# Kernel tuning notes

Hardware: AMD Instinct MI355X
Metric: run time of the kernel (lower is better)

The kernel has to match this reference:

```python
import jax, jax.numpy as jnp
import numpy as np

MASK_VAL = -1e30


def setup_inputs() -> dict:
    key = jax.random.key(0)
    ks = jax.random.split(key, 9)
    B, C, Q, D = 64, 2048, 128, 128
    s = 0.05  # small param init scale (xavier-like)
    return {
        "vfeats": jax.random.normal(ks[0], (B, C, D), jnp.float32),
        "qfeats": jax.random.normal(ks[1], (B, Q, D), jnp.float32),
        "vmask": jnp.ones((B, C), jnp.float32),
        "qmask": jnp.ones((B, Q), jnp.float32),
        "w4C": jax.random.normal(ks[2], (D, 1), jnp.float32) * s,
        "w4Q": jax.random.normal(ks[3], (D, 1), jnp.float32) * s,
        "w4mlu": jax.random.normal(ks[4], (1, 1, D), jnp.float32) * s,
        "cqa_W": jax.random.normal(ks[5], (D, 4 * D), jnp.float32) * s,  # Conv1D k=1 == Linear(4D->D)
        "cqa_b": jnp.zeros((D,), jnp.float32),
        "wp": jax.random.normal(ks[6], (D, 1), jnp.float32) * s,
        "cc_W": jax.random.normal(ks[7], (D, 2 * D), jnp.float32) * s,  # Conv1D k=1 == Linear(2D->D)
        "cc_b": jnp.zeros((D,), jnp.float32),
    }


def reference(vfeats, qfeats, vmask, qmask, w4C, w4Q, w4mlu, cqa_W, cqa_b, wp, cc_W, cc_b):
    # --- CQAttention ---
    # trilinear score: [B, C, Q]  (dropout is identity at inference)
    score = (vfeats @ w4C) \
        + jnp.swapaxes(qfeats @ w4Q, 1, 2) \
        + jnp.einsum('bcd,bqd->bcq', vfeats * w4mlu, qfeats)
    score_ = jax.nn.softmax(score + (1.0 - qmask[:, None, :]) * MASK_VAL, axis=2)   # [B,C,Q]
    score_t = jax.nn.softmax(score + (1.0 - vmask[:, :, None]) * MASK_VAL, axis=1)  # [B,C,Q]
    c2q = score_ @ qfeats                                                           # [B,C,D]
    # q2c = (score_ @ score_t^T) @ context; reassociate to avoid the [B,C,C] matrix
    q2c = score_ @ jnp.einsum('bcq,bcd->bqd', score_t, vfeats)                      # [B,C,D]
    cat = jnp.concatenate([vfeats, c2q, vfeats * c2q, vfeats * q2c], axis=2)        # [B,C,4D]
    feats = cat @ cqa_W.T + cqa_b                                                   # [B,C,D]
    # --- CQConcatenate (weighted pool of query) ---
    alpha = jax.nn.softmax((qfeats @ wp) + (1.0 - qmask[:, :, None]) * MASK_VAL, axis=1)  # [B,Q,1]
    pooled = jnp.einsum('bqd,bq->bd', qfeats, alpha[..., 0])                        # [B,D]
    pooled = jnp.broadcast_to(pooled[:, None, :], feats.shape)                      # [B,C,D]
    out = jnp.concatenate([feats, pooled], axis=2) @ cc_W.T + cc_b                  # [B,C,D]
    return jax.nn.relu(out)
```

## Files before the change

kernel.cpp:

```cpp
#include <hip/hip_runtime.h>
#include <stdint.h>

#define DI __device__ __forceinline__

typedef __attribute__((ext_vector_type(8))) short short8;
typedef __attribute__((ext_vector_type(4))) short short4v;
typedef __attribute__((ext_vector_type(4))) float float4v;
typedef __attribute__((ext_vector_type(2))) float float2v;
typedef __attribute__((ext_vector_type(4))) unsigned int uint4v;
typedef __attribute__((ext_vector_type(2))) unsigned int uint2v;
typedef __attribute__((ext_vector_type(2))) __bf16 bf162;

#define MFMA16(a, b, c) __builtin_amdgcn_mfma_f32_16x16x32_bf16((a), (b), (c), 0, 0, 0)

DI float b2f(short s) {
    uint32_t u = ((uint32_t)(uint16_t)s) << 16;
    float f;
    __builtin_memcpy(&f, &u, 4);
    return f;
}
DI unsigned int cvtpk(float a, float b) {
    bf162 h = __builtin_convertvector((float2v){a, b}, bf162);
    return __builtin_bit_cast(unsigned int, h);
}
DI short f2b(float f) { return (short)__builtin_bit_cast(unsigned short, (__bf16)f); }
DI float u2f(unsigned int u) { return __builtin_bit_cast(float, u); }


__global__ __launch_bounds__(256) void k_packfuse(const float* __restrict__ src, const float* __restrict__ wm,
                                                  const float* __restrict__ wv, const float* __restrict__ mask,
                                                  short* __restrict__ dstA, short* __restrict__ dstT,
                                                  float* __restrict__ dotout, int nkc) {
    __shared__ float St[32 * 133];
    int t = threadIdx.x, kc = blockIdx.x, b = blockIdx.y;
    int rl = t >> 3, sub = t & 7, dseg = sub * 16;
    int grow = (b * nkc + kc) * 32 + rl;
    const float* p = src + ((size_t)grow << 7) + dseg;
    float4v v[4];
#pragma unroll
    for (int g = 0; g < 4; ++g) v[g] = *(const float4v*)(p + g * 4);
    float s = 0.f;
#pragma unroll
    for (int g = 0; g < 4; ++g) {
        float4v wg = *(const float4v*)(wv + dseg + g * 4);
#pragma unroll
        for (int j = 0; j < 4; ++j) s += v[g][j] * wg[j];
    }
#pragma unroll
    for (int off = 1; off < 8; off <<= 1) s += __shfl_xor(s, off, 64);
    if (sub == 0) dotout[grow] = s + (1.f - mask[grow]) * (-1e30f);
#pragma unroll
    for (int g = 0; g < 4; ++g)
#pragma unroll
        for (int j = 0; j < 4; ++j) St[rl * 133 + dseg + g * 4 + j] = v[g][j];
#pragma unroll
    for (int h = 0; h < 2; ++h) {
        int c16 = sub * 2 + h;
        int ks = c16 >> 2, quad = c16 & 3;
        float4v m0 = wm ? *(const float4v*)(wm + c16 * 8) : (float4v){1.f, 1.f, 1.f, 1.f};
        float4v m1 = wm ? *(const float4v*)(wm + c16 * 8 + 4) : (float4v){1.f, 1.f, 1.f, 1.f};
        uint4v ou;
        ou[0] = cvtpk(v[h * 2][0] * m0[0], v[h * 2][1] * m0[1]);
        ou[1] = cvtpk(v[h * 2][2] * m0[2], v[h * 2][3] * m0[3]);
        ou[2] = cvtpk(v[h * 2 + 1][0] * m1[0], v[h * 2 + 1][1] * m1[1]);
        ou[3] = cvtpk(v[h * 2 + 1][2] * m1[2], v[h * 2 + 1][3] * m1[3]);
        int tile = b * (nkc * 2) + kc * 2 + (rl >> 4);
        *(short8*)(dstA + ((size_t)(tile * 4 + ks) << 9) + (quad * 16 + (rl & 15)) * 8) =
            __builtin_bit_cast(short8, ou);
    }
    __syncthreads();
#pragma unroll
    for (int i = 0; i < 2; ++i) {
        int dt = (t >> 6) + i * 4;
        int lane = t & 63, ln = lane & 15, quad = lane >> 4;
        int d = dt * 16 + ln;
        uint4v ou;
#pragma unroll
        for (int wd = 0; wd < 4; ++wd)
            ou[wd] = cvtpk(St[(quad * 8 + 2 * wd) * 133 + d], St[(quad * 8 + 2 * wd + 1) * 133 + d]);
        *(short8*)(dstT + (((size_t)(b * 8 + dt) * nkc + kc) << 9) + lane * 8) = __builtin_bit_cast(short8, ou);
    }
}

__global__ __launch_bounds__(256) void k_packW(const float* __restrict__ wsrc, short* __restrict__ dst) {
    int idx = blockIdx.x * 256 + threadIdx.x;
    int lane = idx & 63, ks = (idx >> 6) & 3, part = (idx >> 8) & 3, nt = idx >> 10;
    const float* p = wsrc + (size_t)(nt * 16 + (lane & 15)) * 512 + part * 128 + ks * 32 + (lane >> 4) * 8;
    float4v a = *(const float4v*)p, b = *(const float4v*)(p + 4);
    uint4v ou;
    ou[0] = cvtpk(a[0], a[1]);
    ou[1] = cvtpk(a[2], a[3]);
    ou[2] = cvtpk(b[0], b[1]);
    ou[3] = cvtpk(b[2], b[3]);
    *(short8*)(dst + (size_t)idx * 8) = __builtin_bit_cast(short8, ou);
}

__global__ __launch_bounds__(256) void k_packWc(const float* __restrict__ wsrc, short* __restrict__ dst) {
    int idx = blockIdx.x * 256 + threadIdx.x;
    int lane = idx & 63, ks = (idx >> 6) & 3, ot = idx >> 8;
    const float* p = wsrc + (size_t)(ot * 16 + (lane & 15)) * 256 + ks * 32 + (lane >> 4) * 8;
    float4v a = *(const float4v*)p, b = *(const float4v*)(p + 4);
    uint4v ou;
    ou[0] = cvtpk(a[0], a[1]);
    ou[1] = cvtpk(a[2], a[3]);
    ou[2] = cvtpk(b[0], b[1]);
    ou[3] = cvtpk(b[2], b[3]);
    *(short8*)(dst + (size_t)idx * 8) = __builtin_bit_cast(short8, ou);
}

__global__ __launch_bounds__(128) void k_pool(const float* __restrict__ qf, const float* __restrict__ qmask,
                                              const float* __restrict__ wp, const float* __restrict__ ccW,
                                              const float* __restrict__ ccb, float* __restrict__ pc) {
    __shared__ float tmp[128], af[128], pooled[128];
    int b = blockIdx.x, t = threadIdx.x;
    const float* qrow = qf + ((size_t)(b * 128 + t) << 7);
    float s = 0.f;
    for (int d = 0; d < 128; ++d) s += qrow[d] * wp[d];
    s += (1.f - qmask[b * 128 + t]) * (-1e30f);
    tmp[t] = s;
    __syncthreads();
    for (int off = 64; off >= 1; off >>= 1) {
        if (t < off) tmp[t] = fmaxf(tmp[t], tmp[t + off]);
        __syncthreads();
    }
    float m = tmp[0];
    __syncthreads();
    float e = __expf(s - m);
    tmp[t] = e;
    __syncthreads();
    for (int off = 64; off >= 1; off >>= 1) {
        if (t < off) tmp[t] += tmp[t + off];
        __syncthreads();
    }
    af[t] = e / tmp[0];
    __syncthreads();
    float p = 0.f;
    for (int q = 0; q < 128; ++q) p += qf[((size_t)(b * 128 + q) << 7) + t] * af[q];
    pooled[t] = p;
    __syncthreads();
    float acc = ccb[t];
    for (int d = 0; d < 128; ++d) acc += pooled[d] * ccW[t * 256 + 128 + d];
    pc[b * 128 + t] = acc;
}

__global__ __launch_bounds__(256) void k_Tacc(const short* __restrict__ vfA, const short* __restrict__ vfT,
                                              const short* __restrict__ qfBW, const float* __restrict__ cvp,
                                              float* __restrict__ Pg, float* __restrict__ Csg) {
    __shared__ short Al[16 * 136];
    __shared__ float Red[4][16][130];
    __shared__ float csred[4][16];
    int tid = threadIdx.x, w = tid >> 6, lane = tid & 63, ln = lane & 15, quad = lane >> 4;
    int id = blockIdx.x;
    int xcd = id & 7, k = id >> 3;
    int g = xcd * 16 + (k & 15);
    int qt = k >> 4;
    int b = g & 63, s = g >> 6;
    short8 bq[4];
#pragma unroll
    for (int ks = 0; ks < 4; ++ks) bq[ks] = *(const short8*)(qfBW + (((size_t)(b * 8 + qt) * 4 + ks) << 9) + lane * 8);
    float4v acc[8];
#pragma unroll
    for (int dt = 0; dt < 8; ++dt) acc[dt] = (float4v){0.f, 0.f, 0.f, 0.f};
    float colacc = 0.f;
    for (int it = 0; it < 8; ++it) {
        int cbase = s * 1024 + it * 128 + w * 32;
        int ct = b * 128 + (cbase >> 4);
        float4v ds[2];
        ds[0] = (float4v){0.f, 0.f, 0.f, 0.f};
        ds[1] = (float4v){0.f, 0.f, 0.f, 0.f};
#pragma unroll
        for (int ks = 0; ks < 4; ++ks) {
#pragma unroll
            for (int mt = 0; mt < 2; ++mt) {
                short8 a = *(const short8*)(vfA + (((size_t)(ct + mt) * 4 + ks) << 9) + lane * 8);
                ds[mt] = MFMA16(a, bq[ks], ds[mt]);
            }
        }
#pragma unroll
        for (int mt = 0; mt < 2; ++mt) {
            float4v cv = *(const float4v*)(cvp + b * 2048 + cbase + mt * 16 + quad * 4);
            float e0 = __expf(ds[mt][0] + cv[0]);
            float e1 = __expf(ds[mt][1] + cv[1]);
            float e2 = __expf(ds[mt][2] + cv[2]);
            float e3 = __expf(ds[mt][3] + cv[3]);
            colacc += e0 + e1 + e2 + e3;
            uint2v eu;
            eu[0] = cvtpk(e0, e1);
            eu[1] = cvtpk(e2, e3);
            *(short4v*)(Al + ln * 136 + w * 32 + mt * 16 + quad * 4) = __builtin_bit_cast(short4v, eu);
        }
        short8 a = *(const short8*)(Al + ln * 136 + w * 32 + quad * 8);
#pragma unroll
        for (int dt = 0; dt < 8; ++dt) {
            short8 bb = *(const short8*)(vfT + (((size_t)(b * 8 + dt) * 64 + s * 32 + it * 4 + w) << 9) + lane * 8);
            acc[dt] = MFMA16(a, bb, acc[dt]);
        }
    }
#pragma unroll
    for (int dt = 0; dt < 8; ++dt)
#pragma unroll
        for (int r = 0; r < 4; ++r) Red[w][quad * 4 + r][dt * 16 + ln] = acc[dt][r];
    float p = colacc;
    p += __shfl_xor(p, 16, 64);
    p += __shfl_xor(p, 32, 64);
    if (lane < 16) csred[w][lane] = p;
    __syncthreads();
    if (tid < 16)
        Csg[((size_t)(s * 64 + b)) * 128 + qt * 16 + tid] =
            csred[0][tid] + csred[1][tid] + csred[2][tid] + csred[3][tid];
    {
        int q = tid >> 4, db = (tid & 15) * 8;
        float4v s0, s1;
#pragma unroll
        for (int j = 0; j < 4; ++j) {
            s0[j] = Red[0][q][db + j] + Red[1][q][db + j] + Red[2][q][db + j] + Red[3][q][db + j];
            s1[j] = Red[0][q][db + 4 + j] + Red[1][q][db + 4 + j] + Red[2][q][db + 4 + j] + Red[3][q][db + 4 + j];
        }
        size_t pb = (((size_t)(s * 64 + b)) * 8 + qt) * 2048 + q * 128 + db;
        *(float4v*)(Pg + pb) = s0;
        *(float4v*)(Pg + pb + 4) = s1;
    }
}

__global__ __launch_bounds__(256) void k_Tcomb(const float* __restrict__ Pg, const float* __restrict__ Csg,
                                               short* __restrict__ Ttf) {
    int idx = blockIdx.x * 256 + threadIdx.x;
    int lane = idx & 63, dt = (idx >> 8) & 7, b = idx >> 11;
    int d = dt * 16 + (lane & 15), q0 = ((idx >> 6) & 3) * 32 + (lane >> 4) * 8;
    float pv[8];
#pragma unroll
    for (int j = 0; j < 8; ++j) {
        int q = q0 + j;
        size_t o0 = ((size_t)(b * 8) + (q >> 4)) * 2048 + (q & 15) * 128 + d;
        size_t o1 = ((size_t)((64 + b) * 8) + (q >> 4)) * 2048 + (q & 15) * 128 + d;
        float cs = Csg[b * 128 + q] + Csg[(64 + b) * 128 + q];
        pv[j] = (Pg[o0] + Pg[o1]) * __builtin_amdgcn_rcpf(cs);
    }
    uint4v ou;
#pragma unroll
    for (int wd = 0; wd < 4; ++wd) ou[wd] = cvtpk(pv[2 * wd], pv[2 * wd + 1]);
    *(short8*)(Ttf + (size_t)idx * 8) = __builtin_bit_cast(short8, ou);
}

__global__ __launch_bounds__(256, 4) void k_out(const short* __restrict__ vfA, const short* __restrict__ qfBW,
                                                const short* __restrict__ qTf, const short* __restrict__ Ttf,
                                                const float* __restrict__ qvp, const short* __restrict__ cqaWp,
                                                const float* __restrict__ cqab, const short* __restrict__ ccWp,
                                                const float* __restrict__ pc, float* __restrict__ out) {
    __shared__ __align__(16) short Sl[64 * 128];
    __shared__ __align__(16) short Xl[64 * 128];
    int tid = threadIdx.x, w = tid >> 6, lane = tid & 63, ln = lane & 15, quad = lane >> 4;
    int jl = ln & 7, hi8 = ln >> 3;
    int id = blockIdx.x;
    int xcd = id & 7, k = id >> 3;
    int b = xcd * 8 + (k & 7);
    int cx = k >> 3;
    int c0 = cx * 64 + w * 16;
    int tt = b * 128 + (c0 >> 4);
    int wbase = w * 2048;
    {
        float4v sc[8];
#pragma unroll
        for (int qt = 0; qt < 8; ++qt) sc[qt] = (float4v){0.f, 0.f, 0.f, 0.f};
#pragma unroll
        for (int ks = 0; ks < 4; ++ks) {
            short8 av = *(const short8*)(vfA + (((size_t)tt * 4 + ks) << 9) + lane * 8);
#pragma unroll
            for (int qt = 0; qt < 8; ++qt) {
                short8 bq = *(const short8*)(qfBW + (((size_t)(b * 8 + qt) * 4 + ks) << 9) + lane * 8);
                sc[qt] = MFMA16(av, bq, sc[qt]);
            }
        }
        float qvl[8];
#pragma unroll
        for (int qt = 0; qt < 8; ++qt) qvl[qt] = qvp[b * 128 + qt * 16 + ln];
#pragma unroll
        for (int r = 0; r < 4; ++r) {
            float x[8], m = -3.4e38f;
#pragma unroll
            for (int qt = 0; qt < 8; ++qt) {
                x[qt] = sc[qt][r] + qvl[qt];
                m = fmaxf(m, x[qt]);
            }
#pragma unroll
            for (int off = 1; off < 16; off <<= 1) m = fmaxf(m, __shfl_xor(m, off, 64));
            float e[8], sm = 0.f;
#pragma unroll
            for (int qt = 0; qt < 8; ++qt) {
                e[qt] = __expf(x[qt] - m);
                sm += e[qt];
            }
#pragma unroll
            for (int off = 1; off < 16; off <<= 1) sm += __shfl_xor(sm, off, 64);
            float inv = __builtin_amdgcn_rcpf(sm);
            int rb = (quad * 4 + r) * 8 + jl;
#pragma unroll
            for (int qp = 0; qp < 4; ++qp) {
                unsigned int u = cvtpk(e[2 * qp] * inv, e[2 * qp + 1] * inv);
                Sl[wbase + qp * 512 + hi8 * 128 + rb] = (short)u;
                Sl[wbase + qp * 512 + (2 + hi8) * 128 + rb] = (short)(u >> 16);
            }
        }
    }
    {
        float4v a2q[8];
#pragma unroll
        for (int dt = 0; dt < 8; ++dt) a2q[dt] = (float4v){0.f, 0.f, 0.f, 0.f};
#pragma unroll
        for (int ks = 0; ks < 4; ++ks) {
            short8 a = *(const short8*)(Sl + wbase + ks * 512 + lane * 8);
#pragma unroll
            for (int dt = 0; dt < 8; ++dt) {
                short8 b1 = *(const short8*)(qTf + (((size_t)(b * 8 + dt) * 4 + ks) << 9) + lane * 8);
                a2q[dt] = MFMA16(a, b1, a2q[dt]);
            }
        }
#pragma unroll
        for (int r = 0; r < 4; ++r) {
            int rb = (quad * 4 + r) * 8 + jl;
#pragma unroll
            for (int dp = 0; dp < 4; ++dp) {
                unsigned int u = cvtpk(a2q[2 * dp][r], a2q[2 * dp + 1][r]);
                Xl[wbase + dp * 512 + hi8 * 128 + rb] = (short)u;
                Xl[wbase + dp * 512 + (2 + hi8) * 128 + rb] = (short)(u >> 16);
            }
        }
    }
    {
        float4v aq2[8];
#pragma unroll
        for (int dt = 0; dt < 8; ++dt) aq2[dt] = (float4v){0.f, 0.f, 0.f, 0.f};
#pragma unroll
        for (int ks = 0; ks < 4; ++ks) {
            short8 a = *(const short8*)(Sl + wbase + ks * 512 + lane * 8);
#pragma unroll
            for (int dt = 0; dt < 8; ++dt) {
                short8 b2 = *(const short8*)(Ttf + (((size_t)(b * 8 + dt) * 4 + ks) << 9) + lane * 8);
                aq2[dt] = MFMA16(a, b2, aq2[dt]);
            }
        }
#pragma unroll
        for (int r = 0; r < 4; ++r) {
            int rb = (quad * 4 + r) * 8 + jl;
#pragma unroll
            for (int dp = 0; dp < 4; ++dp) {
                unsigned int u = cvtpk(aq2[2 * dp][r], aq2[2 * dp + 1][r]);
                Sl[wbase + dp * 512 + hi8 * 128 + rb] = (short)u;
                Sl[wbase + dp * 512 + (2 + hi8) * 128 + rb] = (short)(u >> 16);
            }
        }
    }
    __syncthreads();
    float4v accF[4][2];
#pragma unroll
    for (int ct = 0; ct < 4; ++ct)
#pragma unroll
        for (int nt2 = 0; nt2 < 2; ++nt2) accF[ct][nt2] = (float4v){0.f, 0.f, 0.f, 0.f};
#pragma unroll
    for (int ks = 0; ks < 4; ++ks) {
        short8 avk[4];
#pragma unroll
        for (int ct = 0; ct < 4; ++ct)
            avk[ct] = *(const short8*)(vfA + (((size_t)(b * 128 + cx * 4 + ct) * 4 + ks) << 9) + lane * 8);
#pragma unroll
        for (int part = 0; part < 4; ++part) {
            short8 bwp[2];
#pragma unroll
            for (int nt2 = 0; nt2 < 2; ++nt2)
                bwp[nt2] =
                    *(const short8*)(cqaWp + (((size_t)((w * 2 + nt2) * 4 + part) * 4 + ks) << 9) + lane * 8);
            short8 a[4];
#pragma unroll
            for (int ct = 0; ct < 4; ++ct) {
                int fo = ct * 2048 + ks * 512 + lane * 8;
                if (part == 0) {
                    a[ct] = avk[ct];
                } else if (part == 1) {
                    a[ct] = *(const short8*)(Xl + fo);
                } else {
                    short8 mfr = (part == 2) ? *(const short8*)(Xl + fo) : *(const short8*)(Sl + fo);
                    uint4v ua = __builtin_bit_cast(uint4v, avk[ct]);
                    uint4v um = __builtin_bit_cast(uint4v, mfr);
                    uint4v uo;
#pragma unroll
                    for (int wd = 0; wd < 4; ++wd) {
                        float a0 = u2f(ua[wd] << 16), a1 = u2f(ua[wd] & 0xffff0000u);
                        float m0 = u2f(um[wd] << 16), m1 = u2f(um[wd] & 0xffff0000u);
                        uo[wd] = cvtpk(a0 * m0, a1 * m1);
                    }
                    a[ct] = __builtin_bit_cast(short8, uo);
                }
            }
#pragma unroll
            for (int nt2 = 0; nt2 < 2; ++nt2)
#pragma unroll
                for (int ct = 0; ct < 4; ++ct) accF[ct][nt2] = MFMA16(a[ct], bwp[nt2], accF[ct][nt2]);
        }
    }
    __syncthreads();
    {
        float b0 = cqab[(w * 2) * 16 + ln], b1 = cqab[(w * 2 + 1) * 16 + ln];
#pragma unroll
        for (int ct = 0; ct < 4; ++ct)
#pragma unroll
            for (int r = 0; r < 4; ++r) {
                unsigned int u = cvtpk(accF[ct][0][r] + b0, accF[ct][1][r] + b1);
                int rb = ct * 2048 + w * 512 + (quad * 4 + r) * 8 + jl;
                Sl[rb + hi8 * 128] = (short)u;
                Sl[rb + (2 + hi8) * 128] = (short)(u >> 16);
            }
    }
    __syncthreads();
    float4v accO[4][2];
#pragma unroll
    for (int ct = 0; ct < 4; ++ct)
#pragma unroll
        for (int ot2 = 0; ot2 < 2; ++ot2) accO[ct][ot2] = (float4v){0.f, 0.f, 0.f, 0.f};
#pragma unroll
    for (int ks = 0; ks < 4; ++ks) {
        short8 bwo[2];
#pragma unroll
        for (int ot2 = 0; ot2 < 2; ++ot2)
            bwo[ot2] = *(const short8*)(ccWp + (((size_t)((w * 2 + ot2) * 4 + ks)) << 9) + lane * 8);
        short8 a[4];
#pragma unroll
        for (int ct = 0; ct < 4; ++ct) a[ct] = *(const short8*)(Sl + ct * 2048 + ks * 512 + lane * 8);
#pragma unroll
        for (int ot2 = 0; ot2 < 2; ++ot2)
#pragma unroll
            for (int ct = 0; ct < 4; ++ct) accO[ct][ot2] = MFMA16(a[ct], bwo[ot2], accO[ct][ot2]);
    }
#pragma unroll
    for (int ct = 0; ct < 4; ++ct)
#pragma unroll
        for (int ot2 = 0; ot2 < 2; ++ot2) {
            int o = (w * 2 + ot2) * 16 + ln;
            float pco = pc[b * 128 + o];
#pragma unroll
            for (int r = 0; r < 4; ++r) {
                int c = cx * 64 + ct * 16 + quad * 4 + r;
                out[((size_t)(b * 2048 + c) << 7) + o] = fmaxf(accO[ct][ot2][r] + pco, 0.f);
            }
        }
}

extern "C" void kernel_launch(void* const* d_in, const int* in_sizes, int n_in, void* d_out, int out_size, void* d_ws,
                              size_t ws_size, hipStream_t stream) {
    const float* vf = (const float*)d_in[0];
    const float* qf = (const float*)d_in[1];
    const float* vmask = (const float*)d_in[2];
    const float* qmask = (const float*)d_in[3];
    const float* w4C = (const float*)d_in[4];
    const float* w4Q = (const float*)d_in[5];
    const float* w4mlu = (const float*)d_in[6];
    const float* cqaW = (const float*)d_in[7];
    const float* cqab = (const float*)d_in[8];
    const float* wp = (const float*)d_in[9];
    const float* ccW = (const float*)d_in[10];
    const float* ccb = (const float*)d_in[11];
    float* out = (float*)d_out;
    char* ws = (char*)d_ws;

    size_t o = 0;
    short* vfA = (short*)(ws + o); o += 64ull * 2048 * 128 * 2;
    short* vfT = (short*)(ws + o); o += 64ull * 2048 * 128 * 2;
    short* qfBW = (short*)(ws + o); o += 64ull * 128 * 128 * 2;
    short* qTf = (short*)(ws + o); o += 64ull * 128 * 128 * 2;
    short* Ttf = (short*)(ws + o); o += 64ull * 128 * 128 * 2;
    short* cqaWp = (short*)(ws + o); o += 128ull * 512 * 2;
    short* ccWp = (short*)(ws + o); o += 128ull * 128 * 2;
    float* Pg = (float*)(ws + o); o += 2ull * 64 * 128 * 128 * 4;
    float* Csg = (float*)(ws + o); o += 2ull * 64 * 128 * 4;
    float* cvp = (float*)(ws + o); o += 64ull * 2048 * 4;
    float* qvp = (float*)(ws + o); o += 64ull * 128 * 4;
    float* pc = (float*)(ws + o); o += 64ull * 128 * 4;

    k_packfuse<<<dim3(64, 64), 256, 0, stream>>>(vf, nullptr, w4C, vmask, vfA, vfT, cvp, 64);
    k_packfuse<<<dim3(4, 64), 256, 0, stream>>>(qf, w4mlu, w4Q, qmask, qfBW, qTf, qvp, 4);
    k_packW<<<32, 256, 0, stream>>>(cqaW, cqaWp);
    k_packWc<<<8, 256, 0, stream>>>(ccW, ccWp);
    k_pool<<<64, 128, 0, stream>>>(qf, qmask, wp, ccW, ccb, pc);
    k_Tacc<<<1024, 256, 0, stream>>>(vfA, vfT, qfBW, cvp, Pg, Csg);
    k_Tcomb<<<512, 256, 0, stream>>>(Pg, Csg, Ttf);
    k_out<<<2048, 256, 0, stream>>>(vfA, qfBW, qTf, Ttf, qvp, cqaWp, cqab, ccWp, pc, out);
}
```

Measured before the change: 286.1 us.

## Merge prep kernels into fewer launches and prefetch MFMA operands earlier

The two packfuse launches are merged into one grid that branches on block index, and the weight-pack and pooling kernels are merged into one k_small launch. This cuts the launch count from eight to five. The pooling part now uses 256 threads with vectorized loads and split reductions. In k_Tacc and k_out, the B-operand loads are hoisted ahead of the MFMA loops behind sched_barriers to hide global load latency, at the cost of higher register pressure.

```diff
diff --git a/kernel.cpp b/kernel.cpp
--- a/kernel.cpp
+++ b/kernel.cpp
@@ -23,16 +23,34 @@
     bf162 h = __builtin_convertvector((float2v){a, b}, bf162);
     return __builtin_bit_cast(unsigned int, h);
 }
-DI short f2b(float f) { return (short)__builtin_bit_cast(unsigned short, (__bf16)f); }
 DI float u2f(unsigned int u) { return __builtin_bit_cast(float, u); }
 
 
-__global__ __launch_bounds__(256) void k_packfuse(const float* __restrict__ src, const float* __restrict__ wm,
-                                                  const float* __restrict__ wv, const float* __restrict__ mask,
-                                                  short* __restrict__ dstA, short* __restrict__ dstT,
-                                                  float* __restrict__ dotout, int nkc) {
+__global__ __launch_bounds__(256) void k_packfuse(const float* __restrict__ vf, const float* __restrict__ qf,
+                                                  const float* __restrict__ w4C, const float* __restrict__ w4Q,
+                                                  const float* __restrict__ w4mlu, const float* __restrict__ vmask,
+                                                  const float* __restrict__ qmask, short* __restrict__ vfA,
+                                                  short* __restrict__ vfT, short* __restrict__ qfBW,
+                                                  short* __restrict__ qTf, float* __restrict__ cvp,
+                                                  float* __restrict__ qvp) {
     __shared__ float St[32 * 133];
-    int t = threadIdx.x, kc = blockIdx.x, b = blockIdx.y;
+    int bx = blockIdx.x, b = blockIdx.y;
+    const float* src;
+    const float* wm;
+    const float* wv;
+    const float* mask;
+    short* dstA;
+    short* dstT;
+    float* dotout;
+    int kc, nkc;
+    if (bx < 64) {
+        src = vf; wm = nullptr; wv = w4C; mask = vmask;
+        dstA = vfA; dstT = vfT; dotout = cvp; kc = bx; nkc = 64;
+    } else {
+        src = qf; wm = w4mlu; wv = w4Q; mask = qmask;
+        dstA = qfBW; dstT = qTf; dotout = qvp; kc = bx - 64; nkc = 4;
+    }
+    int t = threadIdx.x;
     int rl = t >> 3, sub = t & 7, dseg = sub * 16;
     int grow = (b * nkc + kc) * 32 + rl;
     const float* p = src + ((size_t)grow << 7) + dseg;
@@ -82,42 +100,52 @@
     }
 }
 
-__global__ __launch_bounds__(256) void k_packW(const float* __restrict__ wsrc, short* __restrict__ dst) {
-    int idx = blockIdx.x * 256 + threadIdx.x;
-    int lane = idx & 63, ks = (idx >> 6) & 3, part = (idx >> 8) & 3, nt = idx >> 10;
-    const float* p = wsrc + (size_t)(nt * 16 + (lane & 15)) * 512 + part * 128 + ks * 32 + (lane >> 4) * 8;
-    float4v a = *(const float4v*)p, b = *(const float4v*)(p + 4);
-    uint4v ou;
-    ou[0] = cvtpk(a[0], a[1]);
-    ou[1] = cvtpk(a[2], a[3]);
-    ou[2] = cvtpk(b[0], b[1]);
-    ou[3] = cvtpk(b[2], b[3]);
-    *(short8*)(dst + (size_t)idx * 8) = __builtin_bit_cast(short8, ou);
-}
-
-__global__ __launch_bounds__(256) void k_packWc(const float* __restrict__ wsrc, short* __restrict__ dst) {
-    int idx = blockIdx.x * 256 + threadIdx.x;
-    int lane = idx & 63, ks = (idx >> 6) & 3, ot = idx >> 8;
-    const float* p = wsrc + (size_t)(ot * 16 + (lane & 15)) * 256 + ks * 32 + (lane >> 4) * 8;
-    float4v a = *(const float4v*)p, b = *(const float4v*)(p + 4);
-    uint4v ou;
-    ou[0] = cvtpk(a[0], a[1]);
-    ou[1] = cvtpk(a[2], a[3]);
-    ou[2] = cvtpk(b[0], b[1]);
-    ou[3] = cvtpk(b[2], b[3]);
-    *(short8*)(dst + (size_t)idx * 8) = __builtin_bit_cast(short8, ou);
-}
-
-__global__ __launch_bounds__(128) void k_pool(const float* __restrict__ qf, const float* __restrict__ qmask,
-                                              const float* __restrict__ wp, const float* __restrict__ ccW,
-                                              const float* __restrict__ ccb, float* __restrict__ pc) {
-    __shared__ float tmp[128], af[128], pooled[128];
-    int b = blockIdx.x, t = threadIdx.x;
-    const float* qrow = qf + ((size_t)(b * 128 + t) << 7);
+__global__ __launch_bounds__(256) void k_small(const float* __restrict__ cqaW, short* __restrict__ cqaWp,
+                                               const float* __restrict__ ccW, short* __restrict__ ccWp,
+                                               const float* __restrict__ qf, const float* __restrict__ qmask,
+                                               const float* __restrict__ wp, const float* __restrict__ ccb,
+                                               float* __restrict__ pc) {
+    int bid = blockIdx.x, t = threadIdx.x;
+    if (bid < 32) {
+        int idx = bid * 256 + t;
+        int lane = idx & 63, ks = (idx >> 6) & 3, part = (idx >> 8) & 3, nt = idx >> 10;
+        const float* p = cqaW + (size_t)(nt * 16 + (lane & 15)) * 512 + part * 128 + ks * 32 + (lane >> 4) * 8;
+        float4v a = *(const float4v*)p, b = *(const float4v*)(p + 4);
+        uint4v ou;
+        ou[0] = cvtpk(a[0], a[1]);
+        ou[1] = cvtpk(a[2], a[3]);
+        ou[2] = cvtpk(b[0], b[1]);
+        ou[3] = cvtpk(b[2], b[3]);
+        *(short8*)(cqaWp + (size_t)idx * 8) = __builtin_bit_cast(short8, ou);
+        return;
+    }
+    if (bid < 40) {
+        int idx = (bid - 32) * 256 + t;
+        int lane = idx & 63, ks = (idx >> 6) & 3, ot = idx >> 8;
+        const float* p = ccW + (size_t)(ot * 16 + (lane & 15)) * 256 + ks * 32 + (lane >> 4) * 8;
+        float4v a = *(const float4v*)p, b = *(const float4v*)(p + 4);
+        uint4v ou;
+        ou[0] = cvtpk(a[0], a[1]);
+        ou[1] = cvtpk(a[2], a[3]);
+        ou[2] = cvtpk(b[0], b[1]);
+        ou[3] = cvtpk(b[2], b[3]);
+        *(short8*)(ccWp + (size_t)idx * 8) = __builtin_bit_cast(short8, ou);
+        return;
+    }
+    __shared__ float tmp[128], af[128], pp[2][128], pooled[128];
+    int b = bid - 40;
+    int q = t >> 1, hf = t & 1;
+    const float* qrow = qf + ((size_t)(b * 128 + q) << 7) + hf * 64;
     float s = 0.f;
-    for (int d = 0; d < 128; ++d) s += qrow[d] * wp[d];
-    s += (1.f - qmask[b * 128 + t]) * (-1e30f);
-    tmp[t] = s;
+#pragma unroll 4
+    for (int d = 0; d < 64; d += 4) {
+        float4v xv = *(const float4v*)(qrow + d);
+        float4v wg = *(const float4v*)(wp + hf * 64 + d);
+        s += xv[0] * wg[0] + xv[1] * wg[1] + xv[2] * wg[2] + xv[3] * wg[3];
+    }
+    s += __shfl_xor(s, 1, 64);
+    s += (1.f - qmask[b * 128 + q]) * (-1e30f);
+    if (hf == 0) tmp[q] = s;
     __syncthreads();
     for (int off = 64; off >= 1; off >>= 1) {
         if (t < off) tmp[t] = fmaxf(tmp[t], tmp[t + off]);
@@ -126,21 +154,31 @@
     float m = tmp[0];
     __syncthreads();
     float e = __expf(s - m);
-    tmp[t] = e;
+    if (hf == 0) tmp[q] = e;
     __syncthreads();
     for (int off = 64; off >= 1; off >>= 1) {
         if (t < off) tmp[t] += tmp[t + off];
         __syncthreads();
     }
-    af[t] = e / tmp[0];
-    __syncthreads();
-    float p = 0.f;
-    for (int q = 0; q < 128; ++q) p += qf[((size_t)(b * 128 + q) << 7) + t] * af[q];
-    pooled[t] = p;
-    __syncthreads();
-    float acc = ccb[t];
-    for (int d = 0; d < 128; ++d) acc += pooled[d] * ccW[t * 256 + 128 + d];
-    pc[b * 128 + t] = acc;
+    if (hf == 0) af[q] = e * __builtin_amdgcn_rcpf(tmp[0]);
+    __syncthreads();
+    {
+        int d = t & 127, qh = t >> 7;
+        float pacc = 0.f;
+        for (int qq = qh * 64; qq < qh * 64 + 64; ++qq) pacc += qf[((size_t)(b * 128 + qq) << 7) + d] * af[qq];
+        pp[qh][d] = pacc;
+    }
+    __syncthreads();
+    if (t < 128) pooled[t] = pp[0][t] + pp[1][t];
+    __syncthreads();
+    {
+        int o = t & 127, dh = t >> 7;
+        float acc = 0.f;
+        for (int d = dh * 64; d < dh * 64 + 64; ++d) acc += pooled[d] * ccW[o * 256 + 128 + d];
+        pp[dh][o] = acc;
+    }
+    __syncthreads();
+    if (t < 128) pc[b * 128 + t] = ccb[t] + pp[0][t] + pp[1][t];
 }
 
 __global__ __launch_bounds__(256) void k_Tacc(const short* __restrict__ vfA, const short* __restrict__ vfT,
@@ -165,6 +203,11 @@
     for (int it = 0; it < 8; ++it) {
         int cbase = s * 1024 + it * 128 + w * 32;
         int ct = b * 128 + (cbase >> 4);
+        short8 bb[4];
+#pragma unroll
+        for (int dt = 0; dt < 4; ++dt)
+            bb[dt] = *(const short8*)(vfT + (((size_t)(b * 8 + dt) * 64 + s * 32 + it * 4 + w) << 9) + lane * 8);
+        __builtin_amdgcn_sched_barrier(0);
         float4v ds[2];
         ds[0] = (float4v){0.f, 0.f, 0.f, 0.f};
         ds[1] = (float4v){0.f, 0.f, 0.f, 0.f};
@@ -191,9 +234,11 @@
         }
         short8 a = *(const short8*)(Al + ln * 136 + w * 32 + quad * 8);
 #pragma unroll
-        for (int dt = 0; dt < 8; ++dt) {
-            short8 bb = *(const short8*)(vfT + (((size_t)(b * 8 + dt) * 64 + s * 32 + it * 4 + w) << 9) + lane * 8);
-            acc[dt] = MFMA16(a, bb, acc[dt]);
+        for (int dt = 0; dt < 4; ++dt) acc[dt] = MFMA16(a, bb[dt], acc[dt]);
+#pragma unroll
+        for (int dt = 4; dt < 8; ++dt) {
+            short8 b2 = *(const short8*)(vfT + (((size_t)(b * 8 + dt) * 64 + s * 32 + it * 4 + w) << 9) + lane * 8);
+            acc[dt] = MFMA16(a, b2, acc[dt]);
         }
     }
 #pragma unroll
@@ -251,6 +296,7 @@
     __shared__ __align__(16) short Xl[64 * 128];
     int tid = threadIdx.x, w = tid >> 6, lane = tid & 63, ln = lane & 15, quad = lane >> 4;
     int jl = ln & 7, hi8 = ln >> 3;
+    const float4v z4 = {0.f, 0.f, 0.f, 0.f};
     int id = blockIdx.x;
     int xcd = id & 7, k = id >> 3;
     int b = xcd * 8 + (k & 7);
@@ -261,19 +307,25 @@
     {
         float4v sc[8];
 #pragma unroll
-        for (int qt = 0; qt < 8; ++qt) sc[qt] = (float4v){0.f, 0.f, 0.f, 0.f};
+        for (int qt = 0; qt < 8; ++qt) sc[qt] = z4;
 #pragma unroll
         for (int ks = 0; ks < 4; ++ks) {
+            short8 bqf[8];
+#pragma unroll
+            for (int qt = 0; qt < 8; ++qt)
+                bqf[qt] = *(const short8*)(qfBW + (((size_t)(b * 8 + qt) * 4 + ks) << 9) + lane * 8);
             short8 av = *(const short8*)(vfA + (((size_t)tt * 4 + ks) << 9) + lane * 8);
 #pragma unroll
-            for (int qt = 0; qt < 8; ++qt) {
-                short8 bq = *(const short8*)(qfBW + (((size_t)(b * 8 + qt) * 4 + ks) << 9) + lane * 8);
-                sc[qt] = MFMA16(av, bq, sc[qt]);
-            }
+            for (int qt = 0; qt < 8; ++qt) sc[qt] = MFMA16(av, bqf[qt], sc[qt]);
         }
         float qvl[8];
 #pragma unroll
         for (int qt = 0; qt < 8; ++qt) qvl[qt] = qvp[b * 128 + qt * 16 + ln];
+        short8 p2[8];
+#pragma unroll
+        for (int dt = 0; dt < 8; ++dt)
+            p2[dt] = *(const short8*)(qTf + (((size_t)(b * 8 + dt) * 4 + 0) << 9) + lane * 8);
+        __builtin_amdgcn_sched_barrier(0);
 #pragma unroll
         for (int r = 0; r < 4; ++r) {
             float x[8], m = -3.4e38f;
@@ -301,20 +353,26 @@
                 Sl[wbase + qp * 512 + (2 + hi8) * 128 + rb] = (short)(u >> 16);
             }
         }
-    }
-    {
+        short8 sa[4];
+#pragma unroll
+        for (int ks = 0; ks < 4; ++ks) sa[ks] = *(const short8*)(Sl + wbase + ks * 512 + lane * 8);
         float4v a2q[8];
 #pragma unroll
-        for (int dt = 0; dt < 8; ++dt) a2q[dt] = (float4v){0.f, 0.f, 0.f, 0.f};
-#pragma unroll
-        for (int ks = 0; ks < 4; ++ks) {
-            short8 a = *(const short8*)(Sl + wbase + ks * 512 + lane * 8);
-#pragma unroll
-            for (int dt = 0; dt < 8; ++dt) {
-                short8 b1 = *(const short8*)(qTf + (((size_t)(b * 8 + dt) * 4 + ks) << 9) + lane * 8);
-                a2q[dt] = MFMA16(a, b1, a2q[dt]);
-            }
-        }
+        for (int dt = 0; dt < 8; ++dt) a2q[dt] = MFMA16(sa[0], p2[dt], z4);
+#pragma unroll
+        for (int ks = 1; ks < 4; ++ks) {
+            short8 bf[8];
+#pragma unroll
+            for (int dt = 0; dt < 8; ++dt)
+                bf[dt] = *(const short8*)(qTf + (((size_t)(b * 8 + dt) * 4 + ks) << 9) + lane * 8);
+#pragma unroll
+            for (int dt = 0; dt < 8; ++dt) a2q[dt] = MFMA16(sa[ks], bf[dt], a2q[dt]);
+        }
+        short8 p3[8];
+#pragma unroll
+        for (int dt = 0; dt < 8; ++dt)
+            p3[dt] = *(const short8*)(Ttf + (((size_t)(b * 8 + dt) * 4 + 0) << 9) + lane * 8);
+        __builtin_amdgcn_sched_barrier(0);
 #pragma unroll
         for (int r = 0; r < 4; ++r) {
             int rb = (quad * 4 + r) * 8 + jl;
@@ -325,19 +383,17 @@
                 Xl[wbase + dp * 512 + (2 + hi8) * 128 + rb] = (short)(u >> 16);
             }
         }
-    }
-    {
         float4v aq2[8];
 #pragma unroll
-        for (int dt = 0; dt < 8; ++dt) aq2[dt] = (float4v){0.f, 0.f, 0.f, 0.f};
-#pragma unroll
-        for (int ks = 0; ks < 4; ++ks) {
-            short8 a = *(const short8*)(Sl + wbase + ks * 512 + lane * 8);
-#pragma unroll
-            for (int dt = 0; dt < 8; ++dt) {
-                short8 b2 = *(const short8*)(Ttf + (((size_t)(b * 8 + dt) * 4 + ks) << 9) + lane * 8);
-                aq2[dt] = MFMA16(a, b2, aq2[dt]);
-            }
+        for (int dt = 0; dt < 8; ++dt) aq2[dt] = MFMA16(sa[0], p3[dt], z4);
+#pragma unroll
+        for (int ks = 1; ks < 4; ++ks) {
+            short8 bf[8];
+#pragma unroll
+            for (int dt = 0; dt < 8; ++dt)
+                bf[dt] = *(const short8*)(Ttf + (((size_t)(b * 8 + dt) * 4 + ks) << 9) + lane * 8);
+#pragma unroll
+            for (int dt = 0; dt < 8; ++dt) aq2[dt] = MFMA16(sa[ks], bf[dt], aq2[dt]);
         }
 #pragma unroll
         for (int r = 0; r < 4; ++r) {
@@ -355,7 +411,7 @@
 #pragma unroll
     for (int ct = 0; ct < 4; ++ct)
 #pragma unroll
-        for (int nt2 = 0; nt2 < 2; ++nt2) accF[ct][nt2] = (float4v){0.f, 0.f, 0.f, 0.f};
+        for (int nt2 = 0; nt2 < 2; ++nt2) accF[ct][nt2] = z4;
 #pragma unroll
     for (int ks = 0; ks < 4; ++ks) {
         short8 avk[4];
@@ -415,7 +471,7 @@
 #pragma unroll
     for (int ct = 0; ct < 4; ++ct)
 #pragma unroll
-        for (int ot2 = 0; ot2 < 2; ++ot2) accO[ct][ot2] = (float4v){0.f, 0.f, 0.f, 0.f};
+        for (int ot2 = 0; ot2 < 2; ++ot2) accO[ct][ot2] = z4;
 #pragma unroll
     for (int ks = 0; ks < 4; ++ks) {
         short8 bwo[2];
@@ -475,11 +531,9 @@
     float* qvp = (float*)(ws + o); o += 64ull * 128 * 4;
     float* pc = (float*)(ws + o); o += 64ull * 128 * 4;
 
-    k_packfuse<<<dim3(64, 64), 256, 0, stream>>>(vf, nullptr, w4C, vmask, vfA, vfT, cvp, 64);
-    k_packfuse<<<dim3(4, 64), 256, 0, stream>>>(qf, w4mlu, w4Q, qmask, qfBW, qTf, qvp, 4);
-    k_packW<<<32, 256, 0, stream>>>(cqaW, cqaWp);
-    k_packWc<<<8, 256, 0, stream>>>(ccW, ccWp);
-    k_pool<<<64, 128, 0, stream>>>(qf, qmask, wp, ccW, ccb, pc);
+    k_packfuse<<<dim3(68, 64), 256, 0, stream>>>(vf, qf, w4C, w4Q, w4mlu, vmask, qmask, vfA, vfT, qfBW, qTf, cvp,
+                                                 qvp);
+    k_small<<<104, 256, 0, stream>>>(cqaW, cqaWp, ccW, ccWp, qf, qmask, wp, ccb, pc);
     k_Tacc<<<1024, 256, 0, stream>>>(vfA, vfT, qfBW, cvp, Pg, Csg);
     k_Tcomb<<<512, 256, 0, stream>>>(Pg, Csg, Ttf);
     k_out<<<2048, 256, 0, stream>>>(vfA, qfBW, qTf, Ttf, qvp, cqaWp, cqab, ccWp, pc, out);
```

Result: faster. 257.4 us (-10.0%).
